# Optimization experiments

Measured on AMD Instinct MI355X. Metric: run time of the kernel, lower is better.

The kernel has to match this reference:

```python
import jax, jax.numpy as jnp
import numpy as np

EMP = 0.1       # threshold from init
EPS = 1e-8      # torch.cosine_similarity eps
ZERO = 9e-15    # replacement value below threshold


def setup_inputs() -> dict:
    key = jax.random.key(0)
    k1, k2 = jax.random.split(key)
    B, N, F = 4, 4096, 64
    x = jax.random.normal(k1, (B, N, F), dtype=jnp.float32)
    w = jax.random.normal(k2, (1, N, F), dtype=jnp.float32)
    return {"x": x, "w": w}


def reference(x, w):
    # x: (B, N, F); w: (1, N, F)
    xw = x * w
    # cosine similarity via normalize + matmul (torch eps clamp on norms)
    nrm = jnp.maximum(jnp.sqrt(jnp.sum(xw * xw, axis=-1, keepdims=True)), EPS)
    xn = xw / nrm                                  # (B, N, F)
    cos = jnp.einsum('bif,bjf->bij', xn, xn)       # (B, N, N)
    return jnp.where(cos > EMP, cos, jnp.asarray(ZERO, cos.dtype))
```

## Files before the change

### kernel.cpp

```cpp
#include <hip/hip_runtime.h>
#include <hip/hip_bf16.h>

typedef _Float16 f16x8 __attribute__((ext_vector_type(8)));
typedef float f32x4 __attribute__((ext_vector_type(4)));

#define N_ROWS 4096
#define F_DIM 64
#define EMPF 0.1f
#define EMPD 0.1
#define ZEROV 9e-15f
#define WINDOW 2e-4f
#define REG_CAP 256u
#define N_REGIONS 4096

__global__ __launch_bounds__(256) void normalize_split_kernel(
    const float* __restrict__ x, const float* __restrict__ w,
    _Float16* __restrict__ hi, _Float16* __restrict__ lo) {
  const int lane = threadIdx.x & 63;
  const int wid = threadIdx.x >> 6;
  const int rg = blockIdx.x * 4 + wid;
  const int n = rg & (N_ROWS - 1);
  const float xv = x[rg * F_DIM + lane];
  const float wv = w[n * F_DIM + lane];
  const float p = xv * wv;
  float s = p * p;
#pragma unroll
  for (int off = 32; off >= 1; off >>= 1) s += __shfl_xor(s, off, 64);
  const float nrm = fmaxf(sqrtf(s), 1e-8f);
  const float xn = p / nrm;
  const _Float16 h = (_Float16)xn;
  const float rem = xn - (float)h;
  hi[rg * F_DIM + lane] = h;
  lo[rg * F_DIM + lane] = (_Float16)rem;
}

__global__ __launch_bounds__(512, 4) void gram_kernel(
    const _Float16* __restrict__ hi, const _Float16* __restrict__ lo,
    float* __restrict__ out, unsigned* __restrict__ cnt,
    unsigned* __restrict__ regions) {
  __shared__ unsigned lds_cnt[8];
  const int lane = threadIdx.x & 63;
  const int wid = threadIdx.x >> 6;
  if (lane == 0) lds_cnt[wid] = 0;

  const int b = blockIdx.y;
  const int row0 = blockIdx.x * 32;
  const int rbase = b * N_ROWS;
  const unsigned rgn = (((unsigned)b * gridDim.x + blockIdx.x) << 3) | (unsigned)wid;
  unsigned* __restrict__ region = regions + (size_t)rgn * REG_CAP;

  const int lr = lane & 15;
  const int lk = (lane >> 4) * 8;

  f16x8 ah[2][2], al[2][2];
#pragma unroll
  for (int g = 0; g < 2; ++g)
#pragma unroll
    for (int kf = 0; kf < 2; ++kf) {
      const int ra = (rbase + row0 + g * 16 + lr) * F_DIM + kf * 32 + lk;
      ah[g][kf] = *(const f16x8*)(hi + ra);
      al[g][kf] = *(const f16x8*)(lo + ra);
    }

  const int r_in = lane & 15;
  const int cb = (lane >> 4) * 4;
  const int colbase = wid * 512;

  int rb = (rbase + colbase + lr) * F_DIM + lk;
  f16x8 bh0 = *(const f16x8*)(hi + rb);
  f16x8 bl0 = *(const f16x8*)(lo + rb);
  f16x8 bh1 = *(const f16x8*)(hi + rb + 32);
  f16x8 bl1 = *(const f16x8*)(lo + rb + 32);

#pragma unroll 1
  for (int j = 0; j < 32; ++j) {
    const int rbn = rb + (j < 31 ? 16 * F_DIM : 0);
    f16x8 nbh0 = *(const f16x8*)(hi + rbn);
    f16x8 nbl0 = *(const f16x8*)(lo + rbn);
    f16x8 nbh1 = *(const f16x8*)(hi + rbn + 32);
    f16x8 nbl1 = *(const f16x8*)(lo + rbn + 32);

    f32x4 acc[2] = {};
#pragma unroll
    for (int g = 0; g < 2; ++g) {
      acc[g] = __builtin_amdgcn_mfma_f32_16x16x32_f16(bh0, ah[g][0], acc[g], 0, 0, 0);
      acc[g] = __builtin_amdgcn_mfma_f32_16x16x32_f16(bh0, al[g][0], acc[g], 0, 0, 0);
      acc[g] = __builtin_amdgcn_mfma_f32_16x16x32_f16(bl0, ah[g][0], acc[g], 0, 0, 0);
      acc[g] = __builtin_amdgcn_mfma_f32_16x16x32_f16(bh1, ah[g][1], acc[g], 0, 0, 0);
      acc[g] = __builtin_amdgcn_mfma_f32_16x16x32_f16(bh1, al[g][1], acc[g], 0, 0, 0);
      acc[g] = __builtin_amdgcn_mfma_f32_16x16x32_f16(bl1, ah[g][1], acc[g], 0, 0, 0);
    }

    const int col = colbase + j * 16 + cb;
#pragma unroll
    for (int g = 0; g < 2; ++g) {
      f32x4 v = acc[g];
      const int row = row0 + g * 16 + r_in;
      const bool near = fabsf(v[0] - EMPF) < WINDOW || fabsf(v[1] - EMPF) < WINDOW ||
                        fabsf(v[2] - EMPF) < WINDOW || fabsf(v[3] - EMPF) < WINDOW;
      if (__builtin_expect(__any((int)near), 0)) {
#pragma unroll
        for (int r = 0; r < 4; ++r) {
          if (fabsf(v[r] - EMPF) < WINDOW) {
            const unsigned pos = atomicAdd(&lds_cnt[wid], 1u);
            if (pos < REG_CAP)
              region[pos] = ((unsigned)b << 24) | ((unsigned)row << 12) | (unsigned)(col + r);
          }
        }
      }
#pragma unroll
      for (int r = 0; r < 4; ++r) v[r] = (v[r] > EMPF) ? v[r] : ZEROV;
      const size_t oi = ((size_t)b << 24) + ((size_t)row << 12) + (size_t)col;
      *(f32x4*)(out + oi) = v;
    }

    bh0 = nbh0; bl0 = nbl0; bh1 = nbh1; bl1 = nbl1;
    rb += 16 * F_DIM;
  }

  if (lane == 0) {
    const unsigned c = lds_cnt[wid];
    cnt[rgn] = c < REG_CAP ? c : REG_CAP;
  }
}

__global__ __launch_bounds__(256) void refine_kernel(
    const float* __restrict__ x, const float* __restrict__ w,
    float* __restrict__ out, const unsigned* __restrict__ cnt,
    const unsigned* __restrict__ regions) {
  const int lane = threadIdx.x & 63;
  const unsigned wg0 = blockIdx.x * (blockDim.x >> 6) + (threadIdx.x >> 6);
  const unsigned nw = gridDim.x * (blockDim.x >> 6);
  for (unsigned rgn = wg0; rgn < N_REGIONS; rgn += nw) {
    const unsigned count = cnt[rgn];
    const unsigned* __restrict__ region = regions + (size_t)rgn * REG_CAP;
    for (unsigned e = 0; e < count; ++e) {
      const unsigned ent = region[e];
      const int b = (int)(ent >> 24);
      const int i = (int)((ent >> 12) & 4095);
      const int j = (int)(ent & 4095);
      const double wi = (double)w[i * F_DIM + lane];
      const double wj = (double)w[j * F_DIM + lane];
      const double xi = (double)x[(b * N_ROWS + i) * F_DIM + lane];
      const double xj = (double)x[(b * N_ROWS + j) * F_DIM + lane];
      const double pi = xi * wi;
      const double pj = xj * wj;
      double si = pi * pi, sj = pj * pj, sij = pi * pj;
#pragma unroll
      for (int off = 32; off >= 1; off >>= 1) {
        si += __shfl_xor(si, off, 64);
        sj += __shfl_xor(sj, off, 64);
        sij += __shfl_xor(sij, off, 64);
      }
      if (lane == 0) {
        const double ni = fmax(sqrt(si), 1e-8);
        const double nj = fmax(sqrt(sj), 1e-8);
        const double c = sij / (ni * nj);
        const double res = (c > EMPD) ? c : (double)ZEROV;
        out[((size_t)b << 24) + ((size_t)i << 12) + (size_t)j] = (float)res;
      }
    }
  }
}

extern "C" void kernel_launch(void* const* d_in, const int* in_sizes, int n_in,
                              void* d_out, int out_size, void* d_ws, size_t ws_size,
                              hipStream_t stream) {
  const float* x = (const float*)d_in[0];
  const float* w = (const float*)d_in[1];
  float* out = (float*)d_out;

  char* ws = (char*)d_ws;
  _Float16* hi = (_Float16*)ws;
  _Float16* lo = (_Float16*)(ws + (size_t)16384 * 64 * 2);
  unsigned* cnt = (unsigned*)(ws + (size_t)4 * 1024 * 1024);
  unsigned* regions = (unsigned*)(ws + (size_t)4 * 1024 * 1024 + 16384);

  normalize_split_kernel<<<4096, 256, 0, stream>>>(x, w, hi, lo);
  gram_kernel<<<dim3(128, 4), 512, 0, stream>>>(hi, lo, out, cnt, regions);
  refine_kernel<<<1024, 256, 0, stream>>>(x, w, out, cnt, regions);
}
```

Measured before the change: 138.6 us.

## Split gram kernel into one 32x32 tile per wave across a 3D grid

```diff
diff --git a/kernel.cpp b/kernel.cpp
--- a/kernel.cpp
+++ b/kernel.cpp
@@ -10,8 +10,8 @@
 #define EMPD 0.1
 #define ZEROV 9e-15f
 #define WINDOW 2e-4f
-#define REG_CAP 256u
-#define N_REGIONS 4096
+#define REG_CAP 16u
+#define N_REGIONS 65536
 
 __global__ __launch_bounds__(256) void normalize_split_kernel(
     const float* __restrict__ x, const float* __restrict__ w,
@@ -34,25 +34,28 @@
   lo[rg * F_DIM + lane] = (_Float16)rem;
 }
 
-__global__ __launch_bounds__(512, 4) void gram_kernel(
+__global__ __launch_bounds__(256, 4) void gram_kernel(
     const _Float16* __restrict__ hi, const _Float16* __restrict__ lo,
     float* __restrict__ out, unsigned* __restrict__ cnt,
     unsigned* __restrict__ regions) {
-  __shared__ unsigned lds_cnt[8];
+  __shared__ unsigned lds_cnt[4];
   const int lane = threadIdx.x & 63;
   const int wid = threadIdx.x >> 6;
   if (lane == 0) lds_cnt[wid] = 0;
 
-  const int b = blockIdx.y;
-  const int row0 = blockIdx.x * 32;
-  const int rbase = b * N_ROWS;
-  const unsigned rgn = (((unsigned)b * gridDim.x + blockIdx.x) << 3) | (unsigned)wid;
+  const int bz = blockIdx.z;
+  const int row0 = blockIdx.x * 64 + (wid >> 1) * 32;
+  const int col0 = blockIdx.y * 64 + (wid & 1) * 32;
+  const int rbase = bz * N_ROWS;
+  const unsigned bid =
+      ((unsigned)bz * gridDim.y + blockIdx.y) * gridDim.x + blockIdx.x;
+  const unsigned rgn = bid * 4u + (unsigned)wid;
   unsigned* __restrict__ region = regions + (size_t)rgn * REG_CAP;
 
   const int lr = lane & 15;
   const int lk = (lane >> 4) * 8;
 
-  f16x8 ah[2][2], al[2][2];
+  f16x8 ah[2][2], al[2][2], bh[2][2], bl[2][2];
 #pragma unroll
   for (int g = 0; g < 2; ++g)
 #pragma unroll
@@ -60,42 +63,34 @@
       const int ra = (rbase + row0 + g * 16 + lr) * F_DIM + kf * 32 + lk;
       ah[g][kf] = *(const f16x8*)(hi + ra);
       al[g][kf] = *(const f16x8*)(lo + ra);
+      const int rb = (rbase + col0 + g * 16 + lr) * F_DIM + kf * 32 + lk;
+      bh[g][kf] = *(const f16x8*)(hi + rb);
+      bl[g][kf] = *(const f16x8*)(lo + rb);
     }
+
+  f32x4 acc[2][2] = {};
+#pragma unroll
+  for (int i = 0; i < 2; ++i)
+#pragma unroll
+    for (int j = 0; j < 2; ++j)
+#pragma unroll
+      for (int kf = 0; kf < 2; ++kf) {
+        acc[i][j] = __builtin_amdgcn_mfma_f32_16x16x32_f16(bh[j][kf], ah[i][kf], acc[i][j], 0, 0, 0);
+        acc[i][j] = __builtin_amdgcn_mfma_f32_16x16x32_f16(bh[j][kf], al[i][kf], acc[i][j], 0, 0, 0);
+        acc[i][j] = __builtin_amdgcn_mfma_f32_16x16x32_f16(bl[j][kf], ah[i][kf], acc[i][j], 0, 0, 0);
+      }
+
+  __builtin_amdgcn_sched_barrier(0);
 
   const int r_in = lane & 15;
   const int cb = (lane >> 4) * 4;
-  const int colbase = wid * 512;
-
-  int rb = (rbase + colbase + lr) * F_DIM + lk;
-  f16x8 bh0 = *(const f16x8*)(hi + rb);
-  f16x8 bl0 = *(const f16x8*)(lo + rb);
-  f16x8 bh1 = *(const f16x8*)(hi + rb + 32);
-  f16x8 bl1 = *(const f16x8*)(lo + rb + 32);
-
-#pragma unroll 1
-  for (int j = 0; j < 32; ++j) {
-    const int rbn = rb + (j < 31 ? 16 * F_DIM : 0);
-    f16x8 nbh0 = *(const f16x8*)(hi + rbn);
-    f16x8 nbl0 = *(const f16x8*)(lo + rbn);
-    f16x8 nbh1 = *(const f16x8*)(hi + rbn + 32);
-    f16x8 nbl1 = *(const f16x8*)(lo + rbn + 32);
-
-    f32x4 acc[2] = {};
 #pragma unroll
-    for (int g = 0; g < 2; ++g) {
-      acc[g] = __builtin_amdgcn_mfma_f32_16x16x32_f16(bh0, ah[g][0], acc[g], 0, 0, 0);
-      acc[g] = __builtin_amdgcn_mfma_f32_16x16x32_f16(bh0, al[g][0], acc[g], 0, 0, 0);
-      acc[g] = __builtin_amdgcn_mfma_f32_16x16x32_f16(bl0, ah[g][0], acc[g], 0, 0, 0);
-      acc[g] = __builtin_amdgcn_mfma_f32_16x16x32_f16(bh1, ah[g][1], acc[g], 0, 0, 0);
-      acc[g] = __builtin_amdgcn_mfma_f32_16x16x32_f16(bh1, al[g][1], acc[g], 0, 0, 0);
-      acc[g] = __builtin_amdgcn_mfma_f32_16x16x32_f16(bl1, ah[g][1], acc[g], 0, 0, 0);
-    }
-
-    const int col = colbase + j * 16 + cb;
+  for (int i = 0; i < 2; ++i)
 #pragma unroll
-    for (int g = 0; g < 2; ++g) {
-      f32x4 v = acc[g];
-      const int row = row0 + g * 16 + r_in;
+    for (int j = 0; j < 2; ++j) {
+      f32x4 v = acc[i][j];
+      const int row = row0 + i * 16 + r_in;
+      const int col = col0 + j * 16 + cb;
       const bool near = fabsf(v[0] - EMPF) < WINDOW || fabsf(v[1] - EMPF) < WINDOW ||
                         fabsf(v[2] - EMPF) < WINDOW || fabsf(v[3] - EMPF) < WINDOW;
       if (__builtin_expect(__any((int)near), 0)) {
@@ -104,19 +99,15 @@
           if (fabsf(v[r] - EMPF) < WINDOW) {
             const unsigned pos = atomicAdd(&lds_cnt[wid], 1u);
             if (pos < REG_CAP)
-              region[pos] = ((unsigned)b << 24) | ((unsigned)row << 12) | (unsigned)(col + r);
+              region[pos] = ((unsigned)bz << 24) | ((unsigned)row << 12) | (unsigned)(col + r);
           }
         }
       }
 #pragma unroll
       for (int r = 0; r < 4; ++r) v[r] = (v[r] > EMPF) ? v[r] : ZEROV;
-      const size_t oi = ((size_t)b << 24) + ((size_t)row << 12) + (size_t)col;
+      const size_t oi = ((size_t)bz << 24) + ((size_t)row << 12) + (size_t)col;
       *(f32x4*)(out + oi) = v;
     }
-
-    bh0 = nbh0; bl0 = nbl0; bh1 = nbh1; bl1 = nbl1;
-    rb += 16 * F_DIM;
-  }
 
   if (lane == 0) {
     const unsigned c = lds_cnt[wid];
@@ -133,8 +124,9 @@
   const unsigned nw = gridDim.x * (blockDim.x >> 6);
   for (unsigned rgn = wg0; rgn < N_REGIONS; rgn += nw) {
     const unsigned count = cnt[rgn];
+    if (count == 0) continue;
     const unsigned* __restrict__ region = regions + (size_t)rgn * REG_CAP;
-    for (unsigned e = 0; e < count; ++e) {
+    for (unsigned e = 0; e < count && e < REG_CAP; ++e) {
       const unsigned ent = region[e];
       const int b = (int)(ent >> 24);
       const int i = (int)((ent >> 12) & 4095);
@@ -174,9 +166,9 @@
   _Float16* hi = (_Float16*)ws;
   _Float16* lo = (_Float16*)(ws + (size_t)16384 * 64 * 2);
   unsigned* cnt = (unsigned*)(ws + (size_t)4 * 1024 * 1024);
-  unsigned* regions = (unsigned*)(ws + (size_t)4 * 1024 * 1024 + 16384);
+  unsigned* regions = (unsigned*)(ws + (size_t)4 * 1024 * 1024 + 262144);
 
   normalize_split_kernel<<<4096, 256, 0, stream>>>(x, w, hi, lo);
-  gram_kernel<<<dim3(128, 4), 512, 0, stream>>>(hi, lo, out, cnt, regions);
+  gram_kernel<<<dim3(64, 64, 4), 256, 0, stream>>>(hi, lo, out, cnt, regions);
   refine_kernel<<<1024, 256, 0, stream>>>(x, w, out, cnt, regions);
 }
```

Measured after the change: 175.8 us. 1.27x slower.
